# Kernel tuning notes

Measured on AMD Instinct MI355X. Metric: run time of the kernel, lower is better.

Reference implementation:

```python
import jax, jax.numpy as jnp
import numpy as np

N, D_FEAT, D, H, L = 2048, 128, 256, 8, 2
DH = D // H
E = 65536
NUM_EDGE_TYPES = 8
MAX_DIST = 10
MAX_DEGREE = 512
D_FF = 4 * D
D_OUT = 128
EPS = 1e-5


def _layernorm(x, g, b):
    mu = jnp.mean(x, axis=-1, keepdims=True)
    var = jnp.mean(jnp.square(x - mu), axis=-1, keepdims=True)
    return (x - mu) * jax.lax.rsqrt(var + EPS) * g + b


def setup_inputs() -> dict:
    key = jax.random.key(0)
    ks = jax.random.split(key, 32)
    inp = {
        "x": jax.random.normal(ks[0], (N, D_FEAT), dtype=jnp.float32),
        "edge_index": jax.random.randint(ks[1], (2, E), 0, N),
        "edge_types": jax.random.randint(ks[2], (E,), 0, NUM_EDGE_TYPES),
        "pos_encoding": jax.random.uniform(ks[3], (N, N), dtype=jnp.float32),
    }
    def xavier(k, shape):
        fan_in, fan_out = shape[0], shape[1]
        lim = float(np.sqrt(6.0 / (fan_in + fan_out)))
        return jax.random.uniform(k, shape, jnp.float32, -lim, lim)
    inp["W_emb"] = xavier(ks[4], (D_FEAT, D)); inp["b_emb"] = jnp.zeros((D,), jnp.float32)
    # stacked per-layer params, stored as [in, out] so y = x @ W + b
    inp["Wq"] = jnp.stack([xavier(jax.random.fold_in(ks[5], l), (D, D)) for l in range(L)])
    inp["Wk"] = jnp.stack([xavier(jax.random.fold_in(ks[6], l), (D, D)) for l in range(L)])
    inp["Wv"] = jnp.stack([xavier(jax.random.fold_in(ks[7], l), (D, D)) for l in range(L)])
    inp["Wo"] = jnp.stack([xavier(jax.random.fold_in(ks[8], l), (D, D)) for l in range(L)])
    for nm in ("bq", "bk", "bv", "bo"):
        inp[nm] = jnp.zeros((L, D), jnp.float32)
    inp["spd_table"] = 0.02 * jax.random.normal(ks[9], (L, MAX_DIST + 1, H), dtype=jnp.float32)
    inp["edge_table"] = 0.02 * jax.random.normal(ks[10], (L, NUM_EDGE_TYPES, H), dtype=jnp.float32)
    inp["din_emb"] = 0.02 * jax.random.normal(ks[11], (L, MAX_DEGREE + 1, D), dtype=jnp.float32)
    inp["dout_emb"] = 0.02 * jax.random.normal(ks[12], (L, MAX_DEGREE + 1, D), dtype=jnp.float32)
    inp["ln1_g"] = jnp.ones((L, D), jnp.float32); inp["ln1_b"] = jnp.zeros((L, D), jnp.float32)
    inp["ln2_g"] = jnp.ones((L, D), jnp.float32); inp["ln2_b"] = jnp.zeros((L, D), jnp.float32)
    inp["W1"] = jnp.stack([xavier(jax.random.fold_in(ks[13], l), (D, D_FF)) for l in range(L)])
    inp["b1"] = jnp.zeros((L, D_FF), jnp.float32)
    inp["W2"] = jnp.stack([xavier(jax.random.fold_in(ks[14], l), (D_FF, D)) for l in range(L)])
    inp["b2"] = jnp.zeros((L, D), jnp.float32)
    inp["W_out"] = xavier(ks[15], (D, D_OUT)); inp["b_out"] = jnp.zeros((D_OUT,), jnp.float32)
    return inp


def _forward(x, edge_index, edge_types, pos_encoding,
             W_emb, b_emb, Wq, bq, Wk, bk, Wv, bv, Wo, bo,
             spd_table, edge_table, din_emb, dout_emb,
             ln1_g, ln1_b, ln2_g, ln2_b, W1, b1, W2, b2, W_out, b_out):
    src, dst = edge_index[0], edge_index[1]
    ones = jnp.ones((E,), jnp.int32)
    deg_out = jnp.clip(jax.ops.segment_sum(ones, src, num_segments=N), 0, MAX_DEGREE)
    deg_in = jnp.clip(jax.ops.segment_sum(ones, dst, num_segments=N), 0, MAX_DEGREE)
    # SPD bucket matrix [N, N] (int), shared across layers
    spd_bucket = jnp.clip(pos_encoding[:, :N] * MAX_DIST + 0.5, 0, MAX_DIST).astype(jnp.int32)

    h = x @ W_emb + b_emb  # node embedding; dropout=0 (eval)
    scale = 1.0 / np.sqrt(DH)
    for l in range(L):
        # centrality encoding
        h = h + din_emb[l][deg_in] + dout_emb[l][deg_out]
        xn = _layernorm(h, ln1_g[l], ln1_b[l])
        q = (xn @ Wq[l] + bq[l]).reshape(N, H, DH).transpose(1, 0, 2)  # [H,N,DH]
        k = (xn @ Wk[l] + bk[l]).reshape(N, H, DH).transpose(1, 0, 2)
        v = (xn @ Wv[l] + bv[l]).reshape(N, H, DH).transpose(1, 0, 2)
        # attention bias [H, N, N]: SPD table gather + per-edge scatter-add
        bias = spd_table[l][spd_bucket].transpose(2, 0, 1)
        e_bias = edge_table[l][edge_types]  # [E, H]
        bias = bias.at[:, src, dst].add(e_bias.T)
        scores = jnp.einsum('hnd,hmd->hnm', q, k) * scale + bias
        attn = jax.nn.softmax(scores, axis=-1)
        attn_out = jnp.einsum('hnm,hmd->hnd', attn, v).transpose(1, 0, 2).reshape(N, D)
        h = h + attn_out @ Wo[l] + bo[l]
        y = _layernorm(h, ln2_g[l], ln2_b[l])
        y = jax.nn.gelu(y @ W1[l] + b1[l], approximate=False) @ W2[l] + b2[l]
        h = h + y
    return h @ W_out + b_out


def reference(x, edge_index, edge_types, pos_encoding,
              W_emb, b_emb, Wq, bq, Wk, bk, Wv, bv, Wo, bo,
              spd_table, edge_table, din_emb, dout_emb,
              ln1_g, ln1_b, ln2_g, ln2_b, W1, b1, W2, b2, W_out, b_out):
    return _forward(x, edge_index, edge_types, pos_encoding,
                    W_emb, b_emb, Wq, bq, Wk, bk, Wv, bv, Wo, bo,
                    spd_table, edge_table, din_emb, dout_emb,
                    ln1_g, ln1_b, ln2_g, ln2_b, W1, b1, W2, b2, W_out, b_out)
```

## Files before the change

### kernel.cpp

```cpp
#include <hip/hip_runtime.h>
#include <math.h>

#define N_NODES 2048
#define D_MODEL 256
#define D_FEAT 128
#define NHEAD 8
#define DH 32
#define NLAYER 2
#define NEDGE 65536
#define D_FF 1024
#define D_OUT 128
#define MAXDEG 512
#define JSPLIT 4

typedef __attribute__((ext_vector_type(8))) short short8;
typedef __attribute__((ext_vector_type(4))) float f32x4;
typedef __attribute__((ext_vector_type(4))) unsigned short u16x4;

__device__ __forceinline__ unsigned short f2bf(float f) {
    unsigned u = __float_as_uint(f);
    unsigned r = (u + 0x7FFFu + ((u >> 16) & 1u)) >> 16;
    return (unsigned short)r;
}

template <int CTRL>
__device__ __forceinline__ float dpp_ror(float x) {
    return __int_as_float(__builtin_amdgcn_update_dpp(0, __float_as_int(x), CTRL, 0xf, 0xf, false));
}

__device__ __forceinline__ void wt_tile(const float* __restrict__ W, unsigned short* __restrict__ Wt,
                                        int K, int Nc, int n0, int k0, int tid,
                                        unsigned short (*tile)[33]) {
    int r = tid >> 3, cg = (tid & 7) * 4;
    float4 w4 = *(const float4*)&W[(size_t)(k0 + r) * Nc + n0 + cg];
    tile[r][cg + 0] = f2bf(w4.x); tile[r][cg + 1] = f2bf(w4.y);
    tile[r][cg + 2] = f2bf(w4.z); tile[r][cg + 3] = f2bf(w4.w);
    __syncthreads();
    int c = tid >> 3, rg = (tid & 7) * 4;
    u16x4 o;
    #pragma unroll
    for (int j = 0; j < 4; j++) o[j] = tile[rg + j][c];
    *(u16x4*)&Wt[(size_t)(n0 + c) * K + k0 + rg] = o;
}

__global__ void mega_prep_kernel(const float* __restrict__ pos, unsigned char* __restrict__ bucket,
                                 unsigned* __restrict__ hist, int* __restrict__ deg_out,
                                 int* __restrict__ deg_in, unsigned* __restrict__ gcursor,
                                 const float* __restrict__ Wq, const float* __restrict__ Wk,
                                 const float* __restrict__ Wv, const float* __restrict__ Wo,
                                 const float* __restrict__ W1, const float* __restrict__ W2,
                                 const float* __restrict__ W_emb, const float* __restrict__ W_out,
                                 const float* __restrict__ bq, const float* __restrict__ bk,
                                 const float* __restrict__ bv,
                                 unsigned short* __restrict__ qkvt, unsigned short* __restrict__ wot,
                                 unsigned short* __restrict__ w1t, unsigned short* __restrict__ w2t,
                                 unsigned short* __restrict__ wembt, unsigned short* __restrict__ woutt,
                                 float* __restrict__ bqkv) {
    __shared__ unsigned short tile[32][33];
    int b = blockIdx.x, tid = threadIdx.x;
    if (b < 4096) {
        int i = b * 256 + tid;
        float4 p = *(const float4*)&pos[(size_t)i * 4];
        unsigned b0 = (unsigned)fminf(fmaxf(p.x * 10.f + 0.5f, 0.f), 10.f);
        unsigned b1 = (unsigned)fminf(fmaxf(p.y * 10.f + 0.5f, 0.f), 10.f);
        unsigned b2 = (unsigned)fminf(fmaxf(p.z * 10.f + 0.5f, 0.f), 10.f);
        unsigned b3 = (unsigned)fminf(fmaxf(p.w * 10.f + 0.5f, 0.f), 10.f);
        ((unsigned*)bucket)[i] = b0 | (b1 << 8) | (b2 << 16) | (b3 << 24);
        if (b < 64) {
            #pragma unroll
            for (int k = 0; k < 4; k++) hist[b * 1024 + k * 256 + tid] = 0;
        } else if (b == 64) {
            #pragma unroll
            for (int k = 0; k < 8; k++) deg_out[k * 256 + tid] = 0;
            #pragma unroll
            for (int k = 0; k < 8; k++) deg_in[k * 256 + tid] = 0;
            if (tid == 0) *gcursor = 0;
        }
        return;
    }
    int bb = b - 4096;
    if (bb < 512) {
        int z = bb >> 6, t = bb & 63;
        int l = z >> 2, which = z & 3;
        const float* W = (which == 0 ? Wq : which == 1 ? Wk : which == 2 ? Wv : Wo) + (size_t)l * 65536;
        unsigned short* dst = (which < 3) ? qkvt + (size_t)l * 196608 + which * 65536
                                          : wot + (size_t)l * 65536;
        wt_tile(W, dst, 256, 256, (t & 7) * 32, (t >> 3) * 32, tid, tile);
    } else if (bb < 1024) {
        int b2 = bb - 512, l = b2 >> 8, t = b2 & 255;
        wt_tile(W1 + (size_t)l * D_MODEL * D_FF, w1t + (size_t)l * D_MODEL * D_FF,
                D_MODEL, D_FF, (t & 31) * 32, (t >> 5) * 32, tid, tile);
    } else if (bb < 1536) {
        int b3 = bb - 1024, l = b3 >> 8, t = b3 & 255;
        wt_tile(W2 + (size_t)l * D_FF * D_MODEL, w2t + (size_t)l * D_FF * D_MODEL,
                D_FF, D_MODEL, (t & 7) * 32, (t >> 3) * 32, tid, tile);
    } else if (bb < 1568) {
        int b4 = bb - 1536;
        wt_tile(W_emb, wembt, D_FEAT, D_MODEL, (b4 & 7) * 32, (b4 >> 3) * 32, tid, tile);
    } else if (bb < 1600) {
        int b5 = bb - 1568;
        wt_tile(W_out, woutt, D_MODEL, D_OUT, (b5 & 3) * 32, (b5 >> 2) * 32, tid, tile);
    } else {
        int i = (bb - 1600) * 256 + tid;
        if (i < NLAYER * 768) {
            int l = i / 768, j = i % 768;
            const float* src = j < 256 ? bq : j < 512 ? bk : bv;
            bqkv[i] = src[l * 256 + (j & 255)];
        }
    }
}

__global__ void degree_hist_kernel(const int* __restrict__ ei,
                                   int* __restrict__ deg_out, int* __restrict__ deg_in,
                                   unsigned* __restrict__ hist) {
    int e = blockIdx.x * 256 + threadIdx.x;
    if (e < NEDGE) {
        int src = ei[e], dst = ei[NEDGE + e];
        atomicAdd(&deg_out[src], 1);
        atomicAdd(&deg_in[dst], 1);
        atomicAdd(&hist[(src >> 6) * 2048 + dst], 1);
    }
}

__global__ void edge_alloc_kernel(const unsigned* __restrict__ hist,
                                  unsigned* __restrict__ offsets, unsigned* __restrict__ cursor,
                                  unsigned* __restrict__ gend, unsigned* __restrict__ gcursor) {
    int g = blockIdx.x;
    int t = threadIdx.x;
    unsigned v = hist[g * 64 + t];
    unsigned inc = v;
    #pragma unroll
    for (int off = 1; off < 64; off <<= 1) {
        unsigned u = __shfl_up(inc, off);
        if (t >= off) inc += u;
    }
    unsigned total = __shfl(inc, 63);
    unsigned base = 0;
    if (t == 63) base = atomicAdd(gcursor, total);
    base = __shfl(base, 63);
    unsigned o = base + inc - v;
    offsets[g * 64 + t] = o;
    cursor[g * 64 + t] = o;
    if (t == 63) gend[g] = base + total;
}

__global__ void edge_scatter_kernel(const int* __restrict__ ei, const int* __restrict__ etypes,
                                    unsigned* __restrict__ cursor, unsigned* __restrict__ packed) {
    int e = blockIdx.x * 256 + threadIdx.x;
    if (e < NEDGE) {
        int src = ei[e], dst = ei[NEDGE + e];
        int key = (src >> 6) * 2048 + dst;
        unsigned pos = atomicAdd(&cursor[key], 1);
        packed[pos] = (unsigned)dst | ((unsigned)(src & 63) << 11) | ((unsigned)etypes[e] << 17);
    }
}

__global__ void centrality_ln_kernel(float* __restrict__ h,
                                     const float* __restrict__ din_l,
                                     const float* __restrict__ dout_l,
                                     const int* __restrict__ deg_in,
                                     const int* __restrict__ deg_out,
                                     const float* __restrict__ g,
                                     const float* __restrict__ b,
                                     unsigned short* __restrict__ y) {
    int row = blockIdx.x;
    int tid = threadIdx.x;
    int di = min(max(deg_in[row], 0), MAXDEG);
    int dn = min(max(deg_out[row], 0), MAXDEG);
    float v = h[row * D_MODEL + tid] + din_l[di * D_MODEL + tid] + dout_l[dn * D_MODEL + tid];
    h[row * D_MODEL + tid] = v;
    __shared__ float red[256];
    red[tid] = v; __syncthreads();
    for (int s = 128; s > 0; s >>= 1) { if (tid < s) red[tid] += red[tid + s]; __syncthreads(); }
    float mu = red[0] * (1.0f / D_MODEL);
    __syncthreads();
    float d = v - mu;
    red[tid] = d * d; __syncthreads();
    for (int s = 128; s > 0; s >>= 1) { if (tid < s) red[tid] += red[tid + s]; __syncthreads(); }
    float rstd = rsqrtf(red[0] * (1.0f / D_MODEL) + 1e-5f);
    y[row * D_MODEL + tid] = f2bf(d * rstd * g[tid] + b[tid]);
}

__global__ void layernorm_kernel(const float* __restrict__ x,
                                 const float* __restrict__ g,
                                 const float* __restrict__ b,
                                 unsigned short* __restrict__ y) {
    int row = blockIdx.x;
    int tid = threadIdx.x;
    float v = x[row * D_MODEL + tid];
    __shared__ float red[256];
    red[tid] = v; __syncthreads();
    for (int s = 128; s > 0; s >>= 1) { if (tid < s) red[tid] += red[tid + s]; __syncthreads(); }
    float mu = red[0] * (1.0f / D_MODEL);
    __syncthreads();
    float d = v - mu;
    red[tid] = d * d; __syncthreads();
    for (int s = 128; s > 0; s >>= 1) { if (tid < s) red[tid] += red[tid + s]; __syncthreads(); }
    float rstd = rsqrtf(red[0] * (1.0f / D_MODEL) + 1e-5f);
    y[row * D_MODEL + tid] = f2bf(d * rstd * g[tid] + b[tid]);
}

template <int ACT, bool RESID, bool OUTBF16, bool AFP32>
__global__ void gemm_mfma_kernel(const void* __restrict__ Av,
                                 const unsigned short* __restrict__ Wt,
                                 const float* __restrict__ bias,
                                 float* __restrict__ C, unsigned short* __restrict__ Cb,
                                 int Nc, int K) {
    __shared__ __align__(16) unsigned short As[32][72];
    __shared__ __align__(16) unsigned short Bs[64][72];
    const unsigned short* A16 = (const unsigned short*)Av;
    const float* A32 = (const float*)Av;
    int tid = threadIdx.x;
    int m0 = blockIdx.y * 32, n0 = blockIdx.x * 64;
    int w = tid >> 6, lane = tid & 63;
    int rg = (w & 1) * 16, cg = (w >> 1) * 32;
    int m = lane & 15, quad = lane >> 4;
    f32x4 acc[2] = {{0.f, 0.f, 0.f, 0.f}, {0.f, 0.f, 0.f, 0.f}};
    int ar = tid >> 3, ac = (tid & 7) * 8;
    uint4 ra; float4 fa0, fa1; uint4 rb0, rb1;
    if (AFP32) {
        fa0 = *(const float4*)&A32[(size_t)(m0 + ar) * K + ac];
        fa1 = *(const float4*)&A32[(size_t)(m0 + ar) * K + ac + 4];
    } else {
        ra = *(const uint4*)&A16[(size_t)(m0 + ar) * K + ac];
    }
    rb0 = *(const uint4*)&Wt[(size_t)(n0 + ar) * K + ac];
    rb1 = *(const uint4*)&Wt[(size_t)(n0 + 32 + ar) * K + ac];
    for (int k0 = 0; k0 < K; k0 += 64) {
        if (AFP32) {
            u16x4 t0 = {f2bf(fa0.x), f2bf(fa0.y), f2bf(fa0.z), f2bf(fa0.w)};
            u16x4 t1 = {f2bf(fa1.x), f2bf(fa1.y), f2bf(fa1.z), f2bf(fa1.w)};
            *(u16x4*)&As[ar][ac] = t0;
            *(u16x4*)&As[ar][ac + 4] = t1;
        } else {
            *(uint4*)&As[ar][ac] = ra;
        }
        *(uint4*)&Bs[ar][ac] = rb0;
        *(uint4*)&Bs[ar + 32][ac] = rb1;
        __syncthreads();
        int kn = k0 + 64;
        if (kn < K) {
            if (AFP32) {
                fa0 = *(const float4*)&A32[(size_t)(m0 + ar) * K + kn + ac];
                fa1 = *(const float4*)&A32[(size_t)(m0 + ar) * K + kn + ac + 4];
            } else {
                ra = *(const uint4*)&A16[(size_t)(m0 + ar) * K + kn + ac];
            }
            rb0 = *(const uint4*)&Wt[(size_t)(n0 + ar) * K + kn + ac];
            rb1 = *(const uint4*)&Wt[(size_t)(n0 + 32 + ar) * K + kn + ac];
        }
        #pragma unroll
        for (int ks = 0; ks < 2; ks++) {
            short8 a = *(const short8*)&As[rg + m][ks * 32 + quad * 8];
            #pragma unroll
            for (int t = 0; t < 2; t++) {
                short8 b = *(const short8*)&Bs[cg + t * 16 + m][ks * 32 + quad * 8];
                acc[t] = __builtin_amdgcn_mfma_f32_16x16x32_bf16(a, b, acc[t], 0, 0, 0);
            }
        }
        __syncthreads();
    }
    #pragma unroll
    for (int t = 0; t < 2; t++) {
        #pragma unroll
        for (int reg = 0; reg < 4; reg++) {
            int row = m0 + rg + quad * 4 + reg;
            int col = n0 + cg + t * 16 + m;
            float val = acc[t][reg] + bias[col];
            if (ACT == 1) val = val * 0.5f * (1.0f + erff(val * 0.7071067811865476f));
            size_t idx = (size_t)row * Nc + col;
            if (RESID) val += C[idx];
            if (OUTBF16) Cb[idx] = f2bf(val);
            else C[idx] = val;
        }
    }
}

__global__ void gemm_qkv_kernel(const unsigned short* __restrict__ A,
                                const unsigned short* __restrict__ Wt,
                                const float* __restrict__ bias,
                                unsigned short* __restrict__ Cb,
                                unsigned short* __restrict__ vbt) {
    const int K = D_MODEL, Nc = 768;
    __shared__ __align__(16) unsigned short As[32][72];
    __shared__ __align__(16) unsigned short Bs[64][72];
    int tid = threadIdx.x;
    int m0 = blockIdx.y * 32, n0 = blockIdx.x * 64;
    int w = tid >> 6, lane = tid & 63;
    int rg = (w & 1) * 16, cg = (w >> 1) * 32;
    int m = lane & 15, quad = lane >> 4;
    f32x4 acc[2] = {{0.f, 0.f, 0.f, 0.f}, {0.f, 0.f, 0.f, 0.f}};
    int ar = tid >> 3, ac = (tid & 7) * 8;
    uint4 ra = *(const uint4*)&A[(size_t)(m0 + ar) * K + ac];
    uint4 rb0 = *(const uint4*)&Wt[(size_t)(n0 + ar) * K + ac];
    uint4 rb1 = *(const uint4*)&Wt[(size_t)(n0 + 32 + ar) * K + ac];
    for (int k0 = 0; k0 < K; k0 += 64) {
        *(uint4*)&As[ar][ac] = ra;
        *(uint4*)&Bs[ar][ac] = rb0;
        *(uint4*)&Bs[ar + 32][ac] = rb1;
        __syncthreads();
        int kn = k0 + 64;
        if (kn < K) {
            ra = *(const uint4*)&A[(size_t)(m0 + ar) * K + kn + ac];
            rb0 = *(const uint4*)&Wt[(size_t)(n0 + ar) * K + kn + ac];
            rb1 = *(const uint4*)&Wt[(size_t)(n0 + 32 + ar) * K + kn + ac];
        }
        #pragma unroll
        for (int ks = 0; ks < 2; ks++) {
            short8 a = *(const short8*)&As[rg + m][ks * 32 + quad * 8];
            #pragma unroll
            for (int t = 0; t < 2; t++) {
                short8 b = *(const short8*)&Bs[cg + t * 16 + m][ks * 32 + quad * 8];
                acc[t] = __builtin_amdgcn_mfma_f32_16x16x32_bf16(a, b, acc[t], 0, 0, 0);
            }
        }
        __syncthreads();
    }
    if (n0 >= 512) {
        #pragma unroll
        for (int t = 0; t < 2; t++) {
            int cl = cg + t * 16 + m;
            float bcol = bias[n0 + cl];
            u16x4 tv;
            #pragma unroll
            for (int reg = 0; reg < 4; reg++) tv[reg] = f2bf(acc[t][reg] + bcol);
            *(u16x4*)&Bs[cl][rg + quad * 4] = tv;
        }
        __syncthreads();
        int rr = tid >> 2, cc = (tid & 3) * 8;
        uint4 o0 = *(const uint4*)&Bs[rr][cc];
        *(uint4*)&vbt[(size_t)(n0 - 512 + rr) * N_NODES + m0 + cc] = o0;
        return;
    }
    #pragma unroll
    for (int t = 0; t < 2; t++) {
        #pragma unroll
        for (int reg = 0; reg < 4; reg++) {
            int row = m0 + rg + quad * 4 + reg;
            int col = n0 + cg + t * 16 + m;
            Cb[(size_t)row * Nc + col] = f2bf(acc[t][reg] + bias[col]);
        }
    }
}

__global__ void gemm_oproj_kernel(const float* __restrict__ part_O,
                                  const float* __restrict__ l_part,
                                  const unsigned short* __restrict__ Wt,
                                  const float* __restrict__ bias,
                                  float* __restrict__ C) {
    __shared__ __align__(16) unsigned short As[32][72];
    __shared__ __align__(16) unsigned short Bs[64][72];
    int tid = threadIdx.x;
    int m0 = blockIdx.y * 32, n0 = blockIdx.x * 64;
    int w = tid >> 6, lane = tid & 63;
    int rg = (w & 1) * 16, cg = (w >> 1) * 32;
    int m = lane & 15, quad = lane >> 4;
    f32x4 acc[2] = {{0.f, 0.f, 0.f, 0.f}, {0.f, 0.f, 0.f, 0.f}};
    int ar = tid >> 3, ac = (tid & 7) * 8;
    int row = m0 + ar;
    for (int k0 = 0; k0 < D_MODEL; k0 += 64) {
        int col = k0 + ac;
        int hh = col >> 5;
        float L = 0.f;
        float o[8] = {0.f, 0.f, 0.f, 0.f, 0.f, 0.f, 0.f, 0.f};
        #pragma unroll
        for (int js = 0; js < JSPLIT; js++) {
            L += l_part[((size_t)js * NHEAD + hh) * N_NODES + row];
            const float* pp = &part_O[((size_t)js * N_NODES + row) * D_MODEL + col];
            float4 p0 = *(const float4*)pp;
            float4 p1 = *(const float4*)(pp + 4);
            o[0] += p0.x; o[1] += p0.y; o[2] += p0.z; o[3] += p0.w;
            o[4] += p1.x; o[5] += p1.y; o[6] += p1.z; o[7] += p1.w;
        }
        float inv = 1.0f / L;
        u16x4 t0, t1;
        #pragma unroll
        for (int j = 0; j < 4; j++) { t0[j] = f2bf(o[j] * inv); t1[j] = f2bf(o[j + 4] * inv); }
        *(u16x4*)&As[ar][ac] = t0;
        *(u16x4*)&As[ar][ac + 4] = t1;
        *(uint4*)&Bs[ar][ac] = *(const uint4*)&Wt[(size_t)(n0 + ar) * D_MODEL + k0 + ac];
        *(uint4*)&Bs[ar + 32][ac] = *(const uint4*)&Wt[(size_t)(n0 + 32 + ar) * D_MODEL + k0 + ac];
        __syncthreads();
        #pragma unroll
        for (int ks = 0; ks < 2; ks++) {
            short8 a = *(const short8*)&As[rg + m][ks * 32 + quad * 8];
            #pragma unroll
            for (int t = 0; t < 2; t++) {
                short8 b = *(const short8*)&Bs[cg + t * 16 + m][ks * 32 + quad * 8];
                acc[t] = __builtin_amdgcn_mfma_f32_16x16x32_bf16(a, b, acc[t], 0, 0, 0);
            }
        }
        __syncthreads();
    }
    #pragma unroll
    for (int t = 0; t < 2; t++) {
        #pragma unroll
        for (int reg = 0; reg < 4; reg++) {
            int orow = m0 + rg + quad * 4 + reg;
            int ocol = n0 + cg + t * 16 + m;
            size_t idx = (size_t)orow * D_MODEL + ocol;
            C[idx] += acc[t][reg] + bias[ocol];
        }
    }
}

__global__ __launch_bounds__(256)
void flash_attn_kernel(const unsigned short* __restrict__ qkvb,
                       const unsigned short* __restrict__ vbt,
                       const unsigned char* __restrict__ bucket,
                       const float* __restrict__ spd_l,
                       const float* __restrict__ et_l,
                       const unsigned* __restrict__ offsets,
                       const unsigned* __restrict__ gend,
                       const unsigned* __restrict__ packed,
                       float* __restrict__ part_O,
                       float* __restrict__ l_part) {
    __shared__ __align__(16) unsigned short ks[64][40];
    __shared__ __align__(16) unsigned short vs[32][72];
    __shared__ __align__(16) float ov[64][68];
    __shared__ float et[8];

    int tid = threadIdx.x;
    int rb = blockIdx.x;
    int i0 = rb * 64;
    int hh = blockIdx.y;
    int js = blockIdx.z;
    int lane = tid & 63;
    if (tid < 8) et[tid] = et_l[tid * NHEAD + hh];
    float spd_reg = spd_l[(lane < 11 ? lane : 10) * NHEAD + hh];

    int w = tid >> 6;
    int m = lane & 15, quad = lane >> 4;
    int r0 = w * 16;
    short8 aq = *(const short8*)&qkvb[(size_t)(i0 + r0 + m) * 768 + hh * DH + quad * 8];
    float l_st[4] = {0.f, 0.f, 0.f, 0.f};
    f32x4 oacc[2] = {{0.f, 0.f, 0.f, 0.f}, {0.f, 0.f, 0.f, 0.f}};
    const float scale = 0.17677669529663687f;
    const int NT = N_NODES / JSPLIT / 64;

    int krow = tid >> 2, kcol = (tid & 3) * 8;
    int vrow = tid >> 3, vcol = (tid & 7) * 8;
    int brow = tid >> 2, bcol = (tid & 3) * 16;

    int jbase = js * (N_NODES / JSPLIT);
    uint4 kpre = *(const uint4*)&qkvb[(size_t)(jbase + krow) * 768 + 256 + hh * DH + kcol];
    uint4 vpre = *(const uint4*)&vbt[(size_t)(hh * DH + vrow) * N_NODES + jbase + vcol];
    uint4 bpre = *(const uint4*)&bucket[(size_t)(i0 + brow) * N_NODES + jbase + bcol];

    for (int jt = 0; jt < NT; jt++) {
        int j0 = jbase + jt * 64;
        *(uint4*)&ks[krow][kcol] = kpre;
        *(uint4*)&vs[vrow][vcol] = vpre;
        {
            const unsigned char* bb = (const unsigned char*)&bpre;
            float fb[16];
            #pragma unroll
            for (int i = 0; i < 16; i++)
                fb[i] = __int_as_float(
                    __builtin_amdgcn_ds_bpermute(((int)bb[i]) << 2, __float_as_int(spd_reg)));
            #pragma unroll
            for (int g = 0; g < 4; g++) {
                f32x4 st = {fb[g * 4], fb[g * 4 + 1], fb[g * 4 + 2], fb[g * 4 + 3]};
                *(f32x4*)&ov[brow][bcol + g * 4] = st;
            }
        }
        __syncthreads();
        if (jt + 1 < NT) {
            int jn = j0 + 64;
            kpre = *(const uint4*)&qkvb[(size_t)(jn + krow) * 768 + 256 + hh * DH + kcol];
            vpre = *(const uint4*)&vbt[(size_t)(hh * DH + vrow) * N_NODES + jn + vcol];
            bpre = *(const uint4*)&bucket[(size_t)(i0 + brow) * N_NODES + jn + bcol];
        }
        {
            unsigned key0 = (unsigned)rb * 2048 + j0;
            unsigned start = offsets[key0], end = gend[key0 >> 6];
            for (unsigned i = start + tid; i < end; i += 256) {
                unsigned p = packed[i];
                atomicAdd(&ov[(p >> 11) & 63][(p & 2047) - j0], et[(p >> 17) & 7]);
            }
        }
        __syncthreads();
        float sv[4][4];
        #pragma unroll
        for (int t = 0; t < 4; t++) {
            short8 bk8 = *(const short8*)&ks[t * 16 + m][quad * 8];
            f32x4 z = {0.f, 0.f, 0.f, 0.f};
            f32x4 sacc = __builtin_amdgcn_mfma_f32_16x16x32_bf16(aq, bk8, z, 0, 0, 0);
            #pragma unroll
            for (int r = 0; r < 4; r++)
                sv[t][r] = __expf(sacc[r] * scale + ov[r0 + quad * 4 + r][t * 16 + m]);
        }
        #pragma unroll
        for (int r = 0; r < 4; r++) {
            float ps = sv[0][r] + sv[1][r] + sv[2][r] + sv[3][r];
            ps += dpp_ror<0x121>(ps);
            ps += dpp_ror<0x122>(ps);
            ps += dpp_ror<0x124>(ps);
            ps += dpp_ror<0x128>(ps);
            l_st[r] += ps;
        }
        #pragma unroll
        for (int t = 0; t < 4; t++)
            #pragma unroll
            for (int r = 0; r < 4; r++)
                ov[r0 + quad * 4 + r][t * 16 + m] = sv[t][r];
        __builtin_amdgcn_s_waitcnt(0xC07F);
        #pragma unroll
        for (int kh = 0; kh < 2; kh++) {
            f32x4 p0 = *(const f32x4*)&ov[r0 + m][kh * 32 + quad * 8];
            f32x4 p1 = *(const f32x4*)&ov[r0 + m][kh * 32 + quad * 8 + 4];
            short8 pa;
            pa[0] = (short)f2bf(p0[0]); pa[1] = (short)f2bf(p0[1]);
            pa[2] = (short)f2bf(p0[2]); pa[3] = (short)f2bf(p0[3]);
            pa[4] = (short)f2bf(p1[0]); pa[5] = (short)f2bf(p1[1]);
            pa[6] = (short)f2bf(p1[2]); pa[7] = (short)f2bf(p1[3]);
            #pragma unroll
            for (int t = 0; t < 2; t++) {
                short8 vb = *(const short8*)&vs[t * 16 + m][kh * 32 + quad * 8];
                oacc[t] = __builtin_amdgcn_mfma_f32_16x16x32_bf16(pa, vb, oacc[t], 0, 0, 0);
            }
        }
        __syncthreads();
    }
    #pragma unroll
    for (int t = 0; t < 2; t++)
        #pragma unroll
        for (int r = 0; r < 4; r++)
            part_O[((size_t)js * N_NODES + i0 + r0 + quad * 4 + r) * D_MODEL + hh * DH + t * 16 + m] =
                oacc[t][r];
    if (m == 0) {
        #pragma unroll
        for (int r = 0; r < 4; r++) {
            int row = i0 + r0 + quad * 4 + r;
            l_part[((size_t)js * NHEAD + hh) * N_NODES + row] = l_st[r];
        }
    }
}

#define WS_ALLOC(type, name, count) \
    type* name = (type*)base; base += (((size_t)(count) * sizeof(type)) + 255) & ~(size_t)255;

extern "C" void kernel_launch(void* const* d_in, const int* in_sizes, int n_in,
                              void* d_out, int out_size, void* d_ws, size_t ws_size,
                              hipStream_t stream) {
    const float* x          = (const float*)d_in[0];
    const int*   edge_index = (const int*)d_in[1];
    const int*   edge_types = (const int*)d_in[2];
    const float* pos        = (const float*)d_in[3];
    const float* W_emb      = (const float*)d_in[4];
    const float* b_emb      = (const float*)d_in[5];
    const float* Wq         = (const float*)d_in[6];
    const float* Wk         = (const float*)d_in[7];
    const float* Wv         = (const float*)d_in[8];
    const float* Wo         = (const float*)d_in[9];
    const float* bq         = (const float*)d_in[10];
    const float* bk         = (const float*)d_in[11];
    const float* bv         = (const float*)d_in[12];
    const float* bo         = (const float*)d_in[13];
    const float* spd_table  = (const float*)d_in[14];
    const float* edge_table = (const float*)d_in[15];
    const float* din_emb    = (const float*)d_in[16];
    const float* dout_emb   = (const float*)d_in[17];
    const float* ln1_g      = (const float*)d_in[18];
    const float* ln1_b      = (const float*)d_in[19];
    const float* ln2_g      = (const float*)d_in[20];
    const float* ln2_b      = (const float*)d_in[21];
    const float* W1         = (const float*)d_in[22];
    const float* b1         = (const float*)d_in[23];
    const float* W2         = (const float*)d_in[24];
    const float* b2         = (const float*)d_in[25];
    const float* W_out      = (const float*)d_in[26];
    const float* b_out      = (const float*)d_in[27];
    float* out = (float*)d_out;

    char* base = (char*)d_ws;
    WS_ALLOC(int, deg_out, N_NODES)
    WS_ALLOC(int, deg_in, N_NODES)
    WS_ALLOC(float, h, N_NODES * D_MODEL)
    WS_ALLOC(unsigned short, xb, N_NODES * D_MODEL)
    WS_ALLOC(unsigned short, qkvb, N_NODES * 768)
    WS_ALLOC(unsigned short, vbt, D_MODEL * N_NODES)
    WS_ALLOC(unsigned short, ffnb, N_NODES * D_FF)
    WS_ALLOC(unsigned char, bucket, (size_t)N_NODES * N_NODES)
    WS_ALLOC(unsigned short, qkvt, NLAYER * 768 * D_MODEL)
    WS_ALLOC(unsigned short, wot, NLAYER * D_MODEL * D_MODEL)
    WS_ALLOC(unsigned short, w1t, NLAYER * D_MODEL * D_FF)
    WS_ALLOC(unsigned short, w2t, NLAYER * D_FF * D_MODEL)
    WS_ALLOC(unsigned short, wembt, D_FEAT * D_MODEL)
    WS_ALLOC(unsigned short, woutt, D_MODEL * D_OUT)
    WS_ALLOC(float, bqkv, NLAYER * 768)
    WS_ALLOC(unsigned, hist, 65536)
    WS_ALLOC(unsigned, offsets, 65536)
    WS_ALLOC(unsigned, cursor, 65536)
    WS_ALLOC(unsigned, gend, 1024)
    WS_ALLOC(unsigned, gcursor, 1)
    WS_ALLOC(unsigned, packed, NEDGE)
    WS_ALLOC(float, part_O, (size_t)JSPLIT * N_NODES * D_MODEL)
    WS_ALLOC(float, l_part, (size_t)JSPLIT * NHEAD * N_NODES)

    mega_prep_kernel<<<5702, 256, 0, stream>>>(pos, bucket, hist, deg_out, deg_in, gcursor,
                                               Wq, Wk, Wv, Wo, W1, W2, W_emb, W_out,
                                               bq, bk, bv, qkvt, wot, w1t, w2t, wembt, woutt, bqkv);
    degree_hist_kernel<<<NEDGE / 256, 256, 0, stream>>>(edge_index, deg_out, deg_in, hist);
    edge_alloc_kernel<<<1024, 64, 0, stream>>>(hist, offsets, cursor, gend, gcursor);
    edge_scatter_kernel<<<NEDGE / 256, 256, 0, stream>>>(edge_index, edge_types, cursor, packed);

    gemm_mfma_kernel<0, false, false, true><<<dim3(D_MODEL / 64, N_NODES / 32), 256, 0, stream>>>(
        x, wembt, b_emb, h, nullptr, D_MODEL, D_FEAT);

    for (int l = 0; l < NLAYER; l++) {
        centrality_ln_kernel<<<N_NODES, 256, 0, stream>>>(
            h, din_emb + (size_t)l * (MAXDEG + 1) * D_MODEL,
            dout_emb + (size_t)l * (MAXDEG + 1) * D_MODEL, deg_in, deg_out,
            ln1_g + l * D_MODEL, ln1_b + l * D_MODEL, xb);

        gemm_qkv_kernel<<<dim3(768 / 64, N_NODES / 32), 256, 0, stream>>>(
            xb, qkvt + (size_t)l * 768 * D_MODEL, bqkv + l * 768, qkvb, vbt);

        flash_attn_kernel<<<dim3(N_NODES / 64, NHEAD, JSPLIT), 256, 0, stream>>>(
            qkvb, vbt, bucket, spd_table + (size_t)l * 11 * NHEAD,
            edge_table + (size_t)l * 8 * NHEAD, offsets, gend, packed, part_O, l_part);

        gemm_oproj_kernel<<<dim3(D_MODEL / 64, N_NODES / 32), 256, 0, stream>>>(
            part_O, l_part, wot + (size_t)l * D_MODEL * D_MODEL, bo + l * D_MODEL, h);

        layernorm_kernel<<<N_NODES, 256, 0, stream>>>(h, ln2_g + l * D_MODEL, ln2_b + l * D_MODEL, xb);

        gemm_mfma_kernel<1, false, true, false><<<dim3(D_FF / 64, N_NODES / 32), 256, 0, stream>>>(
            xb, w1t + (size_t)l * D_MODEL * D_FF, b1 + l * D_FF, nullptr, ffnb, D_FF, D_MODEL);

        gemm_mfma_kernel<0, true, false, false><<<dim3(D_MODEL / 64, N_NODES / 32), 256, 0, stream>>>(
            ffnb, w2t + (size_t)l * D_FF * D_MODEL, b2 + l * D_MODEL, h, nullptr, D_MODEL, D_FF);
    }

    gemm_mfma_kernel<0, false, false, true><<<dim3(D_OUT / 64, N_NODES / 32), 256, 0, stream>>>(
        h, woutt, b_out, out, nullptr, D_OUT, D_MODEL);
}
```

Baseline: 303.5 us.

## Double-buffer K/V tiles and remap bias rows to per-wave ownership in flash attention

K and V shared-memory tiles become double-buffered, so the next tile's stores happen right after the PV MFMAs instead of at the loop head. Bias rows of the ov tile are reassigned so each wave writes the SPD bias only into the rows it consumes itself. This lets the trailing barrier be dropped, leaving two barriers per iteration instead of three. Correctness depends on each wave touching only its own ov rows between the remaining barriers, and the edge atomic scatter still needs the one barrier before it.

After: 300.3 us. No clear change (-1.0%).

```diff
diff --git a/kernel.cpp b/kernel.cpp
--- a/kernel.cpp
+++ b/kernel.cpp
@@ -415,8 +415,8 @@
                        const unsigned* __restrict__ packed,
                        float* __restrict__ part_O,
                        float* __restrict__ l_part) {
-    __shared__ __align__(16) unsigned short ks[64][40];
-    __shared__ __align__(16) unsigned short vs[32][72];
+    __shared__ __align__(16) unsigned short ks[2][64][40];
+    __shared__ __align__(16) unsigned short vs[2][32][72];
     __shared__ __align__(16) float ov[64][68];
     __shared__ float et[8];
 
@@ -440,37 +440,32 @@
 
     int krow = tid >> 2, kcol = (tid & 3) * 8;
     int vrow = tid >> 3, vcol = (tid & 7) * 8;
-    int brow = tid >> 2, bcol = (tid & 3) * 16;
+    int erow = r0 + (lane >> 2);
+    int ecol = (lane & 3) * 16;
 
     int jbase = js * (N_NODES / JSPLIT);
     uint4 kpre = *(const uint4*)&qkvb[(size_t)(jbase + krow) * 768 + 256 + hh * DH + kcol];
     uint4 vpre = *(const uint4*)&vbt[(size_t)(hh * DH + vrow) * N_NODES + jbase + vcol];
-    uint4 bpre = *(const uint4*)&bucket[(size_t)(i0 + brow) * N_NODES + jbase + bcol];
-
+    uint4 bpre = *(const uint4*)&bucket[(size_t)(i0 + erow) * N_NODES + jbase + ecol];
+    *(uint4*)&ks[0][krow][kcol] = kpre;
+    *(uint4*)&vs[0][vrow][vcol] = vpre;
+    {
+        const unsigned char* bb = (const unsigned char*)&bpre;
+        #pragma unroll
+        for (int g = 0; g < 4; g++) {
+            f32x4 st;
+            #pragma unroll
+            for (int i2 = 0; i2 < 4; i2++)
+                st[i2] = __int_as_float(__builtin_amdgcn_ds_bpermute(
+                    ((int)bb[g * 4 + i2]) << 2, __float_as_int(spd_reg)));
+            *(f32x4*)&ov[erow][ecol + g * 4] = st;
+        }
+    }
+
+    int buf = 0;
     for (int jt = 0; jt < NT; jt++) {
         int j0 = jbase + jt * 64;
-        *(uint4*)&ks[krow][kcol] = kpre;
-        *(uint4*)&vs[vrow][vcol] = vpre;
-        {
-            const unsigned char* bb = (const unsigned char*)&bpre;
-            float fb[16];
-            #pragma unroll
-            for (int i = 0; i < 16; i++)
-                fb[i] = __int_as_float(
-                    __builtin_amdgcn_ds_bpermute(((int)bb[i]) << 2, __float_as_int(spd_reg)));
-            #pragma unroll
-            for (int g = 0; g < 4; g++) {
-                f32x4 st = {fb[g * 4], fb[g * 4 + 1], fb[g * 4 + 2], fb[g * 4 + 3]};
-                *(f32x4*)&ov[brow][bcol + g * 4] = st;
-            }
-        }
-        __syncthreads();
-        if (jt + 1 < NT) {
-            int jn = j0 + 64;
-            kpre = *(const uint4*)&qkvb[(size_t)(jn + krow) * 768 + 256 + hh * DH + kcol];
-            vpre = *(const uint4*)&vbt[(size_t)(hh * DH + vrow) * N_NODES + jn + vcol];
-            bpre = *(const uint4*)&bucket[(size_t)(i0 + brow) * N_NODES + jn + bcol];
-        }
+        __syncthreads();
         {
             unsigned key0 = (unsigned)rb * 2048 + j0;
             unsigned start = offsets[key0], end = gend[key0 >> 6];
@@ -479,11 +474,17 @@
                 atomicAdd(&ov[(p >> 11) & 63][(p & 2047) - j0], et[(p >> 17) & 7]);
             }
         }
+        if (jt + 1 < NT) {
+            int jn = j0 + 64;
+            kpre = *(const uint4*)&qkvb[(size_t)(jn + krow) * 768 + 256 + hh * DH + kcol];
+            vpre = *(const uint4*)&vbt[(size_t)(hh * DH + vrow) * N_NODES + jn + vcol];
+            bpre = *(const uint4*)&bucket[(size_t)(i0 + erow) * N_NODES + jn + ecol];
+        }
         __syncthreads();
         float sv[4][4];
         #pragma unroll
         for (int t = 0; t < 4; t++) {
-            short8 bk8 = *(const short8*)&ks[t * 16 + m][quad * 8];
+            short8 bk8 = *(const short8*)&ks[buf][t * 16 + m][quad * 8];
             f32x4 z = {0.f, 0.f, 0.f, 0.f};
             f32x4 sacc = __builtin_amdgcn_mfma_f32_16x16x32_bf16(aq, bk8, z, 0, 0, 0);
             #pragma unroll
@@ -516,11 +517,25 @@
             pa[6] = (short)f2bf(p1[2]); pa[7] = (short)f2bf(p1[3]);
             #pragma unroll
             for (int t = 0; t < 2; t++) {
-                short8 vb = *(const short8*)&vs[t * 16 + m][kh * 32 + quad * 8];
+                short8 vb = *(const short8*)&vs[buf][t * 16 + m][kh * 32 + quad * 8];
                 oacc[t] = __builtin_amdgcn_mfma_f32_16x16x32_bf16(pa, vb, oacc[t], 0, 0, 0);
             }
         }
-        __syncthreads();
+        if (jt + 1 < NT) {
+            *(uint4*)&ks[buf ^ 1][krow][kcol] = kpre;
+            *(uint4*)&vs[buf ^ 1][vrow][vcol] = vpre;
+            const unsigned char* bb = (const unsigned char*)&bpre;
+            #pragma unroll
+            for (int g = 0; g < 4; g++) {
+                f32x4 st;
+                #pragma unroll
+                for (int i2 = 0; i2 < 4; i2++)
+                    st[i2] = __int_as_float(__builtin_amdgcn_ds_bpermute(
+                        ((int)bb[g * 4 + i2]) << 2, __float_as_int(spd_reg)));
+                *(f32x4*)&ov[erow][ecol + g * 4] = st;
+            }
+            buf ^= 1;
+        }
     }
     #pragma unroll
     for (int t = 0; t < 2; t++)
```
